# Kernel optimization log

Hardware: AMD Instinct MI355X
Metric: run time of the kernel (lower is better)

## Reference

```python
import jax, jax.numpy as jnp
import numpy as np

LX, LY = 256, 256
K_CLASSES = 4
N_SWEEPS = 2
N_SITES = LX * LY

# 8-neighborhood offsets (Moore neighborhood), border handled by clipping
_OFFSETS = np.array([[-1, -1], [-1, 0], [-1, 1],
                     [0, -1],           [0, 1],
                     [1, -1],  [1, 0],  [1, 1]], dtype=np.int32)


def setup_inputs() -> dict:
    key = jax.random.key(0)
    k1, k2, k3, k4 = jax.random.split(key, 4)
    X_init = jax.random.randint(k1, (LX, LY), 0, K_CLASSES).astype(jnp.int32)
    perm = jax.random.permutation(k2, jnp.arange(N_SITES)).astype(jnp.int32)
    uniforms = jax.random.uniform(k3, (N_SWEEPS, N_SITES), dtype=jnp.float32)
    beta = jax.random.uniform(k4, (), dtype=jnp.float32) + 0.5  # Potts coupling
    return {"X_init": X_init, "perm": perm, "uniforms": uniforms,
            "beta": beta, "K": K_CLASSES}


def reference(X_init, perm, uniforms, beta, K):
    lx, ly = X_init.shape
    off = jnp.asarray(_OFFSETS)              # (8, 2)
    classes = jnp.arange(K)                  # (K,)

    def update_one_site(X, uv, r):
        u, v = jnp.unravel_index(uv, (lx, ly))
        uu = jnp.clip(u + off[:, 0], 0, lx - 1)   # (8,) neighbor rows
        vv = jnp.clip(v + off[:, 1], 0, ly - 1)   # (8,) neighbor cols
        neigh = X[uu, vv]                          # (8,) dynamic gather
        # Potts potential: p_k proportional to exp(beta * #{neighbors == k})
        counts = (neigh[None, :] == classes[:, None]).sum(axis=1)  # (K,)
        probs = jax.nn.softmax(beta * counts.astype(jnp.float32))  # (K,) sums to 1
        # inverse-CDF categorical sample, as in the original cumsum < r
        x_sample = jnp.count_nonzero(jnp.cumsum(probs) < r)
        return X.at[u, v].set(x_sample.astype(X.dtype))  # scatter write

    def one_sweep(X, rs):
        def body(Xc, inp):
            uv, r = inp
            return update_one_site(Xc, uv, r), None
        X, _ = jax.lax.scan(body, X, (perm, rs))
        return X, None

    X_final, _ = jax.lax.scan(one_sweep, X_init, uniforms)  # N_SWEEPS sweeps
    return X_final
```

## Files before the change

kernel.cpp:

```cpp
#include <hip/hip_runtime.h>
#include <math.h>

#define NSITES 65536
#define WIN 4096
#define NW 16
#define RMAX 64


__device__ __forceinline__ int agg_pos(int v, int* c, int vmax) {
  int pos = 0;
  const int lane = threadIdx.x & 63;
  for (int vv = 1; vv <= vmax; ++vv) {
    unsigned long long m = __ballot(v == vv);
    if (m) {
      int leader = __ffsll((long long)m) - 1;
      int base = 0;
      if (lane == leader) base = atomicAdd(&c[vv], (int)__popcll(m));
      base = __shfl(base, leader);
      if (v == vv) pos = base + (int)__popcll(m & ((1ull << lane) - 1ull));
    }
  }
  return pos;
}

__global__ __launch_bounds__(1024) void GibbsSched_kernel(
    const int* __restrict__ perm, const float* __restrict__ uni,
    uint2* __restrict__ recpk, int* __restrict__ ends) {
  __shared__ unsigned short posg[NSITES];
  __shared__ unsigned short lvl[WIN];
  __shared__ int cnt[RMAX + 1], coff[RMAX + 1];
  __shared__ int chg, bmax;
  const int tid = threadIdx.x;
  const int w = blockIdx.x;
  const int wbase = w * WIN;

  for (int g = tid; g < NSITES / 8; g += 1024)
    ((uint4*)posg)[g] = make_uint4(0u, 0u, 0u, 0u);
  for (int i = tid; i <= RMAX; i += 1024) { cnt[i] = 0; coff[i] = 0; }
  if (tid == 0) bmax = 0;
  __syncthreads();

  int uvk[4];
#pragma unroll
  for (int k = 0; k < 4; ++k) {
    const int lt = tid + k * 1024;
    uvk[k] = perm[wbase + lt];
    posg[uvk[k]] = (unsigned short)(lt + 1);
  }
  __syncthreads();

  unsigned short pred[4][8];
  int myl[4];
#pragma unroll
  for (int k = 0; k < 4; ++k) {
    const int lt = tid + k * 1024;
    const int uv = uvk[k], u = uv >> 8, v = uv & 255;
    const int um = u ? u - 1 : 0, up = u < 255 ? u + 1 : 255;
    const int vm = v ? v - 1 : 0, vp = v < 255 ? v + 1 : 255;
    const int nb8[8] = {(um << 8) | vm, (um << 8) | v, (um << 8) | vp,
                        (u << 8) | vm,                 (u << 8) | vp,
                        (up << 8) | vm, (up << 8) | v, (up << 8) | vp};
#pragma unroll
    for (int j = 0; j < 8; ++j) {
      const int p = posg[nb8[j]];
      pred[k][j] = (p && p - 1 < lt) ? (unsigned short)(p - 1)
                                     : (unsigned short)0xFFFF;
    }
    lvl[lt] = 1;
    myl[k] = 1;
  }
  __syncthreads();

  for (int pass = 0; pass < 128; ++pass) {
    if (tid == 0) chg = 0;
    __syncthreads();
    bool ch = false;
#pragma unroll
    for (int k = 0; k < 4; ++k) {
      int m = 0;
#pragma unroll
      for (int j = 0; j < 8; ++j) {
        const unsigned short p = pred[k][j];
        if (p != 0xFFFF) m = max(m, (int)lvl[p]);
      }
      const int nl = m + 1;
      if (nl != myl[k]) {
        myl[k] = nl;
        lvl[tid + k * 1024] = (unsigned short)nl;
        ch = true;
      }
    }
    if (ch) chg = 1;
    __syncthreads();
    if (chg == 0) break;
  }

#pragma unroll
  for (int k = 0; k < 4; ++k) atomicMax(&bmax, myl[k]);
  __syncthreads();
  const int vmax = bmax;

#pragma unroll
  for (int k = 0; k < 4; ++k) (void)agg_pos(myl[k], cnt, vmax);
  __syncthreads();
  if (tid == 0) {
    int e = 0;
    for (int r = 0; r < RMAX; ++r) {
      coff[r] = e;
      e += cnt[r];
      ends[w * RMAX + r] = e;
    }
  }
  __syncthreads();

#pragma unroll
  for (int k = 0; k < 4; ++k) {
    const int pos = agg_pos(myl[k], coff, vmax);
    const int lt = tid + k * 1024;
    const int gp = wbase + pos;
    recpk[gp] = make_uint2((unsigned)uvk[k],
                           __float_as_uint(uni[wbase + lt]));
    recpk[NSITES + gp] = make_uint2((unsigned)uvk[k],
                                    __float_as_uint(uni[NSITES + wbase + lt]));
  }
}

__device__ __forceinline__ void do_update(unsigned char* cell,
                                          const unsigned int* cellw,
                                          const float4* ctab, unsigned uvv,
                                          float r) {
  const int u = uvv >> 8, v = (int)(uvv & 255u);
  const int um = u ? u - 1 : 0, up = u < 255 ? u + 1 : 255;
  const int vm = v ? v - 1 : 0, vp = v < 255 ? v + 1 : 255;
  const int cb = vm >> 2;
  const int sh0 = (vm & 3) << 3;
  const int shv = (v - vm) << 3;
  const int shp = (vp - vm) << 3;
  int acc = 0;
  {
    const unsigned int* rw = cellw + (um << 6) + cb;
    const unsigned long long wd =
        ((unsigned long long)rw[1] << 32) | (unsigned long long)rw[0];
    const unsigned wl = (unsigned)(wd >> sh0);
    acc += 1 << ((wl & 255u) << 2);
    acc += 1 << (((wl >> shv) & 255u) << 2);
    acc += 1 << (((wl >> shp) & 255u) << 2);
  }
  {
    const unsigned int* rw = cellw + (u << 6) + cb;
    const unsigned long long wd =
        ((unsigned long long)rw[1] << 32) | (unsigned long long)rw[0];
    const unsigned wl = (unsigned)(wd >> sh0);
    acc += 1 << ((wl & 255u) << 2);
    acc += 1 << (((wl >> shp) & 255u) << 2);
  }
  {
    const unsigned int* rw = cellw + (up << 6) + cb;
    const unsigned long long wd =
        ((unsigned long long)rw[1] << 32) | (unsigned long long)rw[0];
    const unsigned wl = (unsigned)(wd >> sh0);
    acc += 1 << ((wl & 255u) << 2);
    acc += 1 << (((wl >> shv) & 255u) << 2);
    acc += 1 << (((wl >> shp) & 255u) << 2);
  }
  const int n0 = acc & 15, n1 = (acc >> 4) & 15, n2 = (acc >> 8) & 15;
  const float4 c = ctab[n0 + 9 * n1 + 81 * n2];
  int cnt = (c.x < r) ? 1 : 0;
  cnt += (c.y < r) ? 1 : 0;
  cnt += (c.z < r) ? 1 : 0;
  cnt += (c.w < r) ? 1 : 0;
  cell[uvv] = (unsigned char)cnt;
}

__global__ __launch_bounds__(1024) void GibbsSampler_90443421319469_kernel(
    const int* __restrict__ Xi, const uint2* __restrict__ recpk,
    const float* __restrict__ betap, const int* __restrict__ ends,
    int* __restrict__ out) {
#pragma clang fp contract(off)
  __shared__ __align__(16) unsigned int cellw[NSITES / 4];
  __shared__ float4 ctab[732];
  __shared__ int lend[NW * RMAX];
  unsigned char* cell = (unsigned char*)cellw;
  const int tid = threadIdx.x;
  const float beta = betap[0];

  for (int g = tid; g < NSITES / 4; g += 1024) {
    int4 x = ((const int4*)Xi)[g];
    cellw[g] = (unsigned)(x.x & 255) | ((unsigned)(x.y & 255) << 8) |
               ((unsigned)(x.z & 255) << 16) | ((unsigned)(x.w & 255) << 24);
  }
  lend[tid] = ends[tid];
  for (int t = tid; t < 729; t += 1024) {
    const int n0 = t % 9, n1 = (t / 9) % 9, n2 = t / 81;
    const int n3 = 8 - n0 - n1 - n2;
    float4 val = make_float4(2.f, 2.f, 2.f, 2.f);
    if (n3 >= 0) {
      const int mx = max(max(n0, n1), max(n2, n3));
      const float xm = beta * (float)mx;
      const float x0 = beta * (float)n0;
      const float x1 = beta * (float)n1;
      const float x2 = beta * (float)n2;
      const float x3 = beta * (float)n3;
      const float e0 = (float)exp((double)(x0 - xm));
      const float e1 = (float)exp((double)(x1 - xm));
      const float e2 = (float)exp((double)(x2 - xm));
      const float e3 = (float)exp((double)(x3 - xm));
      const float s = ((e0 + e1) + e2) + e3;
      const float c0 = e0 / s;
      const float c1 = c0 + e1 / s;
      const float c2 = c1 + e2 / s;
      const float c3 = c2 + e3 / s;
      val = make_float4(c0, c1, c2, c3);
    }
    ctab[t] = val;
  }
  __syncthreads();

  for (int w = 0; w < 2 * NW; ++w) {
    const int ww = w & (NW - 1);
    const int sw = w >> 4;
    const uint2* rp = recpk + sw * NSITES + ww * WIN;
    const int* le = &lend[ww * RMAX];

    int nb = 0, ne = le[1];
    uint2 cur = make_uint2(0u, 0u);
    if (tid < ne) cur = rp[tid];

    for (int rd = 1; rd < RMAX; ++rd) {
      const int b = nb, e = ne;
      if (b >= WIN) break;
      nb = e;
      ne = (rd + 1 < RMAX) ? le[rd + 1] : e;
      uint2 nxt = make_uint2(0u, 0u);
      if (nb + tid < ne) nxt = rp[nb + tid];
      if (b + tid < e) do_update(cell, cellw, ctab, cur.x, __uint_as_float(cur.y));
      for (int i = b + tid + 1024; i < e; i += 1024) {
        const uint2 rc = rp[i];
        do_update(cell, cellw, ctab, rc.x, __uint_as_float(rc.y));
      }
      __syncthreads();
      cur = nxt;
    }
  }

  for (int g = tid; g < NSITES / 4; g += 1024) {
    const unsigned p = cellw[g];
    int4 o;
    o.x = (int)(p & 255u);
    o.y = (int)((p >> 8) & 255u);
    o.z = (int)((p >> 16) & 255u);
    o.w = (int)((p >> 24) & 255u);
    ((int4*)out)[g] = o;
  }
}

extern "C" void kernel_launch(void* const* d_in, const int* in_sizes, int n_in,
                              void* d_out, int out_size, void* d_ws,
                              size_t ws_size, hipStream_t stream) {
  const int* Xi = (const int*)d_in[0];
  const int* perm = (const int*)d_in[1];
  const float* uni = (const float*)d_in[2];
  const float* beta = (const float*)d_in[3];
  int* out = (int*)d_out;

  char* ws = (char*)d_ws;
  uint2* recpk = (uint2*)ws;
  int* ends = (int*)(ws + 2 * NSITES * 8);

  GibbsSched_kernel<<<dim3(NW), dim3(1024), 0, stream>>>(perm, uni, recpk,
                                                         ends);
  GibbsSampler_90443421319469_kernel<<<dim3(1), dim3(1024), 0, stream>>>(
      Xi, recpk, beta, ends, out);
}
```

Baseline: 230.7 us.

## Preload whole window records into registers with double-buffered prefetch

Each thread now loads all 4096 records of a window into registers (4 per thread) before processing it, and prefetches the next window's records into a second register set while the current window runs. Rounds then select from the register-held records by range check instead of issuing a global load per round. This removes per-round global-memory latency on the serial critical path. The cost is more register pressure and four predicated update slots per round, with only one or two typically active.

```diff
diff --git a/kernel.cpp b/kernel.cpp
--- a/kernel.cpp
+++ b/kernel.cpp
@@ -172,6 +172,27 @@
   cell[uvv] = (unsigned char)cnt;
 }
 
+__device__ __forceinline__ void run_rounds(unsigned char* cell,
+                                           const unsigned int* cellw,
+                                           const float4* ctab, const int* le,
+                                           const uint2 (&R)[4], int tid) {
+  int b = 0, e = le[1];
+  for (int rd = 1; rd < RMAX; ++rd) {
+    if (b >= WIN) break;
+    const int nb = e;
+    const int ne = (rd + 1 < RMAX) ? le[rd + 1] : e;
+#pragma unroll
+    for (int k = 0; k < 4; ++k) {
+      const int s = tid + (k << 10);
+      if (s >= b && s < e)
+        do_update(cell, cellw, ctab, R[k].x, __uint_as_float(R[k].y));
+    }
+    __syncthreads();
+    b = nb;
+    e = ne;
+  }
+}
+
 __global__ __launch_bounds__(1024) void GibbsSampler_90443421319469_kernel(
     const int* __restrict__ Xi, const uint2* __restrict__ recpk,
     const float* __restrict__ betap, const int* __restrict__ ends,
@@ -183,6 +204,10 @@
   unsigned char* cell = (unsigned char*)cellw;
   const int tid = threadIdx.x;
   const float beta = betap[0];
+
+  uint2 ra[4], rb[4];
+#pragma unroll
+  for (int k = 0; k < 4; ++k) ra[k] = recpk[tid + (k << 10)];
 
   for (int g = tid; g < NSITES / 4; g += 1024) {
     int4 x = ((const int4*)Xi)[g];
@@ -218,28 +243,21 @@
 
   for (int w = 0; w < 2 * NW; ++w) {
     const int ww = w & (NW - 1);
-    const int sw = w >> 4;
-    const uint2* rp = recpk + sw * NSITES + ww * WIN;
     const int* le = &lend[ww * RMAX];
-
-    int nb = 0, ne = le[1];
-    uint2 cur = make_uint2(0u, 0u);
-    if (tid < ne) cur = rp[tid];
-
-    for (int rd = 1; rd < RMAX; ++rd) {
-      const int b = nb, e = ne;
-      if (b >= WIN) break;
-      nb = e;
-      ne = (rd + 1 < RMAX) ? le[rd + 1] : e;
-      uint2 nxt = make_uint2(0u, 0u);
-      if (nb + tid < ne) nxt = rp[nb + tid];
-      if (b + tid < e) do_update(cell, cellw, ctab, cur.x, __uint_as_float(cur.y));
-      for (int i = b + tid + 1024; i < e; i += 1024) {
-        const uint2 rc = rp[i];
-        do_update(cell, cellw, ctab, rc.x, __uint_as_float(rc.y));
-      }
-      __syncthreads();
-      cur = nxt;
+    const int wn = w + 1;
+    const uint2* rpn = recpk + (wn >> 4) * NSITES + (wn & (NW - 1)) * WIN;
+    if ((w & 1) == 0) {
+      if (wn < 2 * NW) {
+#pragma unroll
+        for (int k = 0; k < 4; ++k) rb[k] = rpn[tid + (k << 10)];
+      }
+      run_rounds(cell, cellw, ctab, le, ra, tid);
+    } else {
+      if (wn < 2 * NW) {
+#pragma unroll
+        for (int k = 0; k < 4; ++k) ra[k] = rpn[tid + (k << 10)];
+      }
+      run_rounds(cell, cellw, ctab, le, rb, tid);
     }
   }
 
```

Measured after the change: 213.8 us. -7.3%, faster.
